# Optimization experiments

Measured on AMD Instinct MI355X. Metric: run time of the kernel, lower is better.

Reference implementation:

```python
import jax, jax.numpy as jnp
import numpy as np

P, M, N, H, B, E, K = 50, 512, 1024, 256, 8, 400, 5
ALPHA_MAX, TAU_MAX, RHO_MAX, ETA_MAX = 0.01, 1.0, 1.0, 1.0
LEAK = 0.01  # F.leaky_relu default slope


def _lrelu(x):
    return jnp.where(x >= 0, x, LEAK * x)


def _layernorm(x, g, b, eps=1e-5):
    mu = jnp.mean(x, axis=-1, keepdims=True)
    var = jnp.mean((x - mu) ** 2, axis=-1, keepdims=True)
    return (x - mu) * jax.lax.rsqrt(var + eps) * g + b


def setup_inputs() -> dict:
    ks = iter(jax.random.split(jax.random.key(0), 16))

    def w(fin, fout):
        return jax.random.normal(next(ks), (fin, fout), jnp.float32) * np.float32(np.sqrt(2.0 / (fin + fout)))

    H4 = 4 * H
    inp = {
        'A': jax.random.normal(next(ks), (1, P, M, N), jnp.float32) * 0.05,
        'b': jax.random.normal(next(ks), (B, P, M, 1), jnp.float32),
        'W1': w(2 * N, H), 'b1': jnp.zeros(H), 'bn1_s': jnp.ones(H), 'bn1_t': jnp.zeros(H),
        'W2': w(H, 2 * H), 'b2': jnp.zeros(2 * H), 'bn2_s': jnp.ones(2 * H), 'bn2_t': jnp.zeros(2 * H),
        'W3': w(2 * H, H4), 'b3': jnp.zeros(H4), 'bn3_s': jnp.ones(H4), 'bn3_t': jnp.zeros(H4),
        'W4': w(H4, H4), 'b4': jnp.zeros(H4), 'bn4_s': jnp.ones(H4), 'bn4_t': jnp.zeros(H4),
        'W5': w(H4, H4), 'b5': jnp.zeros(H4), 'bn5_s': jnp.ones(H4), 'bn5_t': jnp.zeros(H4),
        'ln_g': jnp.ones(H4), 'ln_b': jnp.zeros(H4),
        'Wd1': w(P * H4, H4), 'bd1': jnp.zeros(H4), 'lnd1_g': jnp.ones(H4), 'lnd1_b': jnp.zeros(H4),
        'Wd2': w(H4, 2 * H), 'bd2': jnp.zeros(2 * H), 'lnd2_g': jnp.ones(2 * H), 'lnd2_b': jnp.zeros(2 * H),
        'Wd3': w(2 * H, H), 'bd3': jnp.zeros(H), 'lnd3_g': jnp.ones(H), 'lnd3_b': jnp.zeros(H),
        'Wfc': w(H, 4) * 0.1, 'bfc': jnp.zeros(4),
        'edge_index': jax.random.randint(next(ks), (2, E), 0, P),
    }
    return inp


def reference(A, b, W1, b1, bn1_s, bn1_t, W2, b2, bn2_s, bn2_t, W3, b3, bn3_s, bn3_t,
              W4, b4, bn4_s, bn4_t, W5, b5, bn5_s, bn5_t, ln_g, ln_b,
              Wd1, bd1, lnd1_g, lnd1_b, Wd2, bd2, lnd2_g, lnd2_b, Wd3, bd3, lnd3_g, lnd3_b,
              Wfc, bfc, edge_index):
    A0 = A[0]                                             # [P,M,N]
    AtA = jnp.einsum('pmi,pmj->pij', A0, A0)              # [P,N,N]  (compute_Atx(A))
    Atb = jnp.einsum('pmn,bpm->bpn', A0, b[..., 0])[..., None]  # [B,P,N,1]

    src, dst = edge_index[0], edge_index[1]
    ones_e = jnp.ones((E,), A.dtype)
    # sum_neighbors: out-degree of each node p, shape broadcastable to [B,P,1,1]
    sum_nb = jax.ops.segment_sum(ones_e, src, num_segments=P)[None, :, None, None]

    # GCNConv normalization with self loops: norm_ij = deg_i^-1/2 * deg_j^-1/2
    sl = jnp.arange(P)
    src_a = jnp.concatenate([src, sl])
    dst_a = jnp.concatenate([dst, sl])
    deg = jax.ops.segment_sum(jnp.ones((E + P,), A.dtype), dst_a, num_segments=P)
    dinv = jax.lax.rsqrt(deg)
    coef = (dinv[src_a] * dinv[dst_a])[:, None]           # [E+P,1]

    convs = [(W1, b1, bn1_s, bn1_t), (W2, b2, bn2_s, bn2_t), (W3, b3, bn3_s, bn3_t),
             (W4, b4, bn4_s, bn4_t), (W5, b5, bn5_s, bn5_t)]

    def gconv(x, W, bias):                                # x: [P,Cin]
        xw = x @ W
        return jax.ops.segment_sum(xw[src_a] * coef, dst_a, num_segments=P) + bias

    def encode_one(feat):                                 # feat: [P,2N]
        x = feat
        for (W, bias, s, t) in convs:
            # leaky_relu -> BatchNorm1d (eval: affine scale/shift) -> dropout (eval: id)
            x = _lrelu(gconv(x, W, bias)) * s + t
        return _layernorm(x, ln_g, ln_b).reshape(-1)      # [P*4H]

    enc = jax.vmap(encode_one)

    y = jnp.zeros((B, P, N, 1), A.dtype)
    U = jnp.zeros_like(y)
    delta = jnp.zeros_like(y)
    Ys = []
    for k in range(K):
        AtAy = jnp.einsum('pij,bpj->bpi', AtA, y[..., 0])[..., None]  # [B,P,N,1]
        feat = jnp.concatenate([AtAy, Atb], axis=2)[..., 0]           # [B,P,2N]
        code = enc(feat)                                              # [B,P*4H]
        h = _lrelu(_layernorm(code @ Wd1 + bd1, lnd1_g, lnd1_b))
        h = _lrelu(_layernorm(h @ Wd2 + bd2, lnd2_g, lnd2_b))
        h = _lrelu(_layernorm(h @ Wd3 + bd3, lnd3_g, lnd3_b))
        hyp = jnp.clip(jax.nn.sigmoid(h @ Wfc + bfc), 1e-4, 0.99).reshape(B, 4, 1, 1, 1)
        alpha = hyp[:, 0] * ALPHA_MAX
        tau = hyp[:, 1] * TAU_MAX
        rho = hyp[:, 2] * RHO_MAX
        eta = hyp[:, 3] * ETA_MAX
        g = AtAy - Atb + jnp.sign(y) * tau + U * sum_nb + delta * rho
        mg = max(30.0, 100.0 - k)
        g = jnp.clip(g, -mg, mg)
        mv = max(10.0, 200.0 - k * 3)
        y = jnp.clip(y - alpha * g, -mv, mv)
        # compute_delta: for each directed edge (s,d): delta[s]+= (y_s-y_d); delta[d]-= (y_s-y_d)
        diff = y[:, src] - y[:, dst]                                  # [B,E,N,1]
        delta = jnp.zeros_like(y).at[:, src].add(diff).at[:, dst].add(-diff)
        U = jnp.clip(U + delta * eta, -mv, mv)
        Ys.append(y)
    return jnp.stack(Ys)                                              # [K,B,P,N,1]
```

## Files before the change

kernel.cpp:

```cpp
#include <hip/hip_runtime.h>

#define PP 50
#define MM 512
#define NN 1024

constexpr size_t F_ATB   = 0;
constexpr size_t F_ATAY  = F_ATB   + 409600;
constexpr size_t F_Y     = F_ATAY  + 409600;
constexpr size_t F_U     = F_Y     + 409600;
constexpr size_t F_DELTA = F_U     + 409600;
constexpr size_t F_BT    = F_DELTA + 409600;
constexpr size_t F_AYT   = F_BT    + 204800;
constexpr size_t F_ZA    = F_AYT   + 204800;
constexpr size_t F_ZB    = F_ZA    + 458752;
constexpr size_t F_X0    = F_ZB    + 458752;
constexpr size_t F_X1    = F_X0    + 409600;
constexpr size_t F_CODET = F_X1    + 409600;
constexpr size_t F_PART  = F_CODET + 409600;
constexpr size_t F_DPART2= F_PART  + 3670016;
constexpr size_t F_H1    = F_DPART2+ 32768;
constexpr size_t F_H2    = F_H1    + 8192;
constexpr size_t F_H3    = F_H2    + 4096;
constexpr size_t F_HYP   = F_H3    + 2048;
constexpr size_t F_GCCO  = F_HYP   + 64;
constexpr size_t F_SUMNB = F_GCCO  + 512;
constexpr size_t F_END   = F_SUMNB + 64;

__device__ __forceinline__ float lrelu(float v) { return v >= 0.f ? v : 0.01f * v; }

__device__ __forceinline__ void bred2(float& s1, float& s2, float* sm) {
  #pragma unroll
  for (int off = 32; off > 0; off >>= 1) {
    s1 += __shfl_down(s1, off);
    s2 += __shfl_down(s2, off);
  }
  int w = threadIdx.x >> 6, l = threadIdx.x & 63;
  if (l == 0) { sm[w] = s1; sm[4 + w] = s2; }
  __syncthreads();
  s1 = sm[0] + sm[1] + sm[2] + sm[3];
  s2 = sm[4] + sm[5] + sm[6] + sm[7];
}

__global__ __launch_bounds__(512) void ksetup(const int* __restrict__ ei, float* sumnb,
                                              float* gccoef, int* gcoff, int* gcsrc,
                                              int* nbroff, int* nbridx) {
  __shared__ int cin[PP];
  __shared__ int cou[PP];
  __shared__ float sdinv[PP];
  __shared__ int goff[PP + 1], noff[PP + 1];
  int t = threadIdx.x;
  const int* src = ei;
  const int* dst = ei + 400;
  if (t < PP) { cin[t] = 0; cou[t] = 0; }
  __syncthreads();
  if (t < 400) {
    atomicAdd(&cou[src[t]], 1);
    atomicAdd(&cin[dst[t]], 1);
  }
  __syncthreads();
  if (t < PP) {
    sdinv[t] = rsqrtf((float)(cin[t] + 1));
    sumnb[t] = (float)cou[t];
  }
  __syncthreads();
  if (t == 0) {
    goff[0] = 0; noff[0] = 0;
    for (int p = 0; p < PP; ++p) {
      goff[p + 1] = goff[p] + cin[p] + 1;
      noff[p + 1] = noff[p] + cin[p] + cou[p];
    }
  }
  __syncthreads();
  if (t <= PP) { gcoff[t] = goff[t]; nbroff[t] = noff[t]; }
  if (t < 400) {
    int d = dst[t], s = src[t];
    int slot = 0;
    for (int e = 0; e < t; ++e) slot += (dst[e] == d) ? 1 : 0;
    int pos = goff[d] + slot;
    gcsrc[pos] = s;
    gccoef[pos] = sdinv[s] * sdinv[d];
  }
  if (t < PP) {
    int pos = goff[t] + cin[t];
    gcsrc[pos] = t;
    gccoef[pos] = sdinv[t] * sdinv[t];
  }
  if (t < 400) {
    int s = src[t], d = dst[t];
    int so = 0, si = 0;
    for (int e = 0; e < t; ++e) {
      so += (src[e] == s) ? 1 : 0;
      si += (dst[e] == d) ? 1 : 0;
    }
    nbridx[noff[s] + so] = d;
    nbridx[noff[d] + cou[d] + si] = s;
  }
}

__global__ __launch_bounds__(256) void kbt(const float* __restrict__ b, float* __restrict__ bt) {
  int i = blockIdx.x * 256 + threadIdx.x;
  int bb = i / (PP * MM);
  int r = i - bb * (PP * MM);
  bt[r * 8 + bb] = b[i];
}

__global__ __launch_bounds__(256) void katz(const float* __restrict__ A, const float* __restrict__ q,
                                            float* __restrict__ outv) {
  __shared__ float red[4][64][8];
  int nb = blockIdx.x, p = blockIdx.y, t = threadIdx.x;
  int ln = t & 63, mg = t >> 6;
  int n = nb * 64 + ln;
  float acc[8] = {0, 0, 0, 0, 0, 0, 0, 0};
  const float* ap = A + ((size_t)p * MM + mg * 128) * NN + n;
  const float* qp = q + ((size_t)p * MM + mg * 128) * 8;
  for (int m0 = 0; m0 < 128; m0 += 8) {
    float av[8];
    #pragma unroll
    for (int u = 0; u < 8; ++u) av[u] = ap[(size_t)(m0 + u) * NN];
    #pragma unroll
    for (int u = 0; u < 8; ++u) {
      #pragma unroll
      for (int bb = 0; bb < 8; ++bb) acc[bb] += av[u] * qp[(m0 + u) * 8 + bb];
    }
  }
  #pragma unroll
  for (int bb = 0; bb < 8; ++bb) red[mg][ln][bb] = acc[bb];
  __syncthreads();
  if (mg == 0) {
    #pragma unroll
    for (int bb = 0; bb < 8; ++bb) {
      float v = red[0][ln][bb] + red[1][ln][bb] + red[2][ln][bb] + red[3][ln][bb];
      outv[((size_t)bb * PP + p) * NN + n] = v;
    }
  }
}

__global__ __launch_bounds__(256) void kay(const float* __restrict__ A, const float* __restrict__ y,
                                           float* __restrict__ ayt) {
  __shared__ __align__(16) float sy[8][NN];
  int p = blockIdx.x, mb = blockIdx.y, t = threadIdx.x;
  #pragma unroll
  for (int bb = 0; bb < 8; ++bb)
    for (int n = t; n < NN; n += 256) sy[bb][n] = y[(bb * PP + p) * NN + n];
  __syncthreads();
  int w = t >> 6, l = t & 63;
  int mbase = mb * 64 + w * 16;
  for (int i = 0; i < 8; ++i) {
    int m0 = mbase + 2 * i, m1 = m0 + 1;
    float acc0[8] = {0, 0, 0, 0, 0, 0, 0, 0};
    float acc1[8] = {0, 0, 0, 0, 0, 0, 0, 0};
    const float* a0p = A + ((size_t)p * MM + m0) * NN;
    const float* a1p = a0p + NN;
    #pragma unroll
    for (int jj = 0; jj < 4; ++jj) {
      int n0 = 4 * l + 256 * jj;
      float4 a0 = *(const float4*)(a0p + n0);
      float4 a1 = *(const float4*)(a1p + n0);
      #pragma unroll
      for (int bb = 0; bb < 8; ++bb) {
        float4 yv = *(const float4*)&sy[bb][n0];
        acc0[bb] += a0.x * yv.x + a0.y * yv.y + a0.z * yv.z + a0.w * yv.w;
        acc1[bb] += a1.x * yv.x + a1.y * yv.y + a1.z * yv.z + a1.w * yv.w;
      }
    }
    #pragma unroll
    for (int off = 32; off > 0; off >>= 1) {
      #pragma unroll
      for (int bb = 0; bb < 8; ++bb) {
        acc0[bb] += __shfl_down(acc0[bb], off);
        acc1[bb] += __shfl_down(acc1[bb], off);
      }
    }
    if (l == 0) {
      #pragma unroll
      for (int bb = 0; bb < 8; ++bb) {
        ayt[((size_t)p * MM + m0) * 8 + bb] = acc0[bb];
        ayt[((size_t)p * MM + m1) * 8 + bb] = acc1[bb];
      }
    }
  }
}

__global__ __launch_bounds__(256) void kgatherX(const float* __restrict__ x, float* __restrict__ z,
                                                int Cin, const int* __restrict__ gcoff,
                                                const int* __restrict__ gcsrc,
                                                const float* __restrict__ gccoef) {
  int r = blockIdx.x, cc = blockIdx.y, t = threadIdx.x;
  int c = cc * 256 + t;
  size_t zi = (size_t)r * Cin + c;
  if (r >= 400) { z[zi] = 0.f; return; }
  int b = r / 50, p = r - b * 50;
  float acc = 0.f;
  int o0 = gcoff[p], o1 = gcoff[p + 1];
  for (int idx = o0; idx < o1; ++idx)
    acc += gccoef[idx] * x[((size_t)b * 50 + gcsrc[idx]) * Cin + c];
  z[zi] = acc;
}

__global__ __launch_bounds__(256) void kgemm(const float* __restrict__ X, const float* __restrict__ W,
                                             float* __restrict__ part, int K, int C, int krange) {
  int cb = blockIdx.x, rb = blockIdx.y, s = blockIdx.z;
  int t = threadIdx.x;
  __shared__ __align__(16) float As[16][64];
  __shared__ __align__(16) float Bs[16][68];
  int rbase = rb * 64, cbase = cb * 64;
  int k0 = s * krange, kend = k0 + krange;
  float acc[4][4] = {};
  int tx = t & 15, ty = t >> 4;
  int lrow = t >> 2, lk = (t & 3) * 4;
  int brow = t >> 4, bc = (t & 15) * 4;
  for (int k = k0; k < kend; k += 16) {
    float4 av = *(const float4*)(X + (size_t)(rbase + lrow) * K + k + lk);
    As[lk + 0][lrow] = av.x;
    As[lk + 1][lrow] = av.y;
    As[lk + 2][lrow] = av.z;
    As[lk + 3][lrow] = av.w;
    *(float4*)&Bs[brow][bc] = *(const float4*)(W + (size_t)(k + brow) * C + cbase + bc);
    __syncthreads();
    #pragma unroll
    for (int kk = 0; kk < 16; ++kk) {
      float4 a = *(const float4*)&As[kk][ty * 4];
      float4 b = *(const float4*)&Bs[kk][tx * 4];
      float aa[4] = {a.x, a.y, a.z, a.w};
      float bb[4] = {b.x, b.y, b.z, b.w};
      #pragma unroll
      for (int i = 0; i < 4; ++i)
        #pragma unroll
        for (int j = 0; j < 4; ++j) acc[i][j] += aa[i] * bb[j];
    }
    __syncthreads();
  }
  #pragma unroll
  for (int i = 0; i < 4; ++i) {
    int r = rbase + ty * 4 + i;
    *(float4*)&part[((size_t)s * 448 + r) * C + cbase + tx * 4] =
        make_float4(acc[i][0], acc[i][1], acc[i][2], acc[i][3]);
  }
}

__global__ __launch_bounds__(256) void kgemmC(const float* __restrict__ XA, const float* __restrict__ XB,
                                              const float* __restrict__ W, float* __restrict__ part,
                                              int C, int krange, int koff) {
  int cb = blockIdx.x, rb = blockIdx.y, s = blockIdx.z;
  int t = threadIdx.x;
  __shared__ __align__(16) float As[16][64];
  __shared__ __align__(16) float Bs[16][68];
  int rbase = rb * 64, cbase = cb * 64;
  int k0 = koff + s * krange, kend = k0 + krange;
  float acc[4][4] = {};
  int tx = t & 15, ty = t >> 4;
  int lrow = t >> 2, lk = (t & 3) * 4;
  int brow = t >> 4, bc = (t & 15) * 4;
  for (int k = k0; k < kend; k += 16) {
    int r = rbase + lrow;
    const float* xp = (k < 1024) ? (XA + (size_t)r * 1024 + k)
                                 : (XB + (size_t)r * 1024 + (k - 1024));
    float4 av = *(const float4*)(xp + lk);
    As[lk + 0][lrow] = av.x;
    As[lk + 1][lrow] = av.y;
    As[lk + 2][lrow] = av.z;
    As[lk + 3][lrow] = av.w;
    *(float4*)&Bs[brow][bc] = *(const float4*)(W + (size_t)(k + brow) * C + cbase + bc);
    __syncthreads();
    #pragma unroll
    for (int kk = 0; kk < 16; ++kk) {
      float4 a = *(const float4*)&As[kk][ty * 4];
      float4 b = *(const float4*)&Bs[kk][tx * 4];
      float aa[4] = {a.x, a.y, a.z, a.w};
      float bb[4] = {b.x, b.y, b.z, b.w};
      #pragma unroll
      for (int i = 0; i < 4; ++i)
        #pragma unroll
        for (int j = 0; j < 4; ++j) acc[i][j] += aa[i] * bb[j];
    }
    __syncthreads();
  }
  #pragma unroll
  for (int i = 0; i < 4; ++i) {
    int r = rbase + ty * 4 + i;
    *(float4*)&part[((size_t)s * 448 + r) * C + cbase + tx * 4] =
        make_float4(acc[i][0], acc[i][1], acc[i][2], acc[i][3]);
  }
}

template <int NCH, bool LASTLN>
__global__ __launch_bounds__(256) void kredE(const float* __restrict__ part, int S,
                                             const float* __restrict__ bias,
                                             const float* __restrict__ bns,
                                             const float* __restrict__ bnt,
                                             float* __restrict__ xout,
                                             const float* __restrict__ lng,
                                             const float* __restrict__ lnb,
                                             float* __restrict__ codet) {
  __shared__ float smr[8];
  constexpr int C = NCH * 256;
  int r = blockIdx.x, t = threadIdx.x;
  float vals[NCH];
  #pragma unroll
  for (int ch = 0; ch < NCH; ++ch) {
    int c = ch * 256 + t;
    float acc = 0.f;
    const float* pp = part + (size_t)r * C + c;
    #pragma unroll 4
    for (int s = 0; s < S; ++s) acc += pp[(size_t)s * 448 * C];
    float v = lrelu(acc + bias[c]);
    vals[ch] = v * bns[c] + bnt[c];
  }
  if (!LASTLN) {
    #pragma unroll
    for (int ch = 0; ch < NCH; ++ch)
      xout[(size_t)r * C + ch * 256 + t] = vals[ch];
  } else {
    float s1 = 0.f, s2 = 0.f;
    #pragma unroll
    for (int ch = 0; ch < NCH; ++ch) { s1 += vals[ch]; s2 += vals[ch] * vals[ch]; }
    bred2(s1, s2, smr);
    float mu = s1 / (float)C;
    float var = s2 / (float)C - mu * mu;
    float rs = rsqrtf(var + 1e-5f);
    int b = r / 50, p = r - b * 50;
    #pragma unroll
    for (int ch = 0; ch < NCH; ++ch) {
      int c = ch * 256 + t;
      codet[((size_t)p * C + c) * 8 + b] = (vals[ch] - mu) * rs * lng[c] + lnb[c];
    }
  }
}

__global__ __launch_bounds__(256) void kwd1(const float* __restrict__ W,
                                            const float* __restrict__ in_t,
                                            float* __restrict__ dpart) {
  int t = threadIdx.x, s = blockIdx.x;
  int k0 = s * 200;
  float4 acc[8];
  #pragma unroll
  for (int b = 0; b < 8; ++b) acc[b] = make_float4(0.f, 0.f, 0.f, 0.f);
  const float* wp = W + (size_t)k0 * 1024 + 4 * t;
  const float* qp = in_t + (size_t)k0 * 8;
  for (int k = 0; k < 200; k += 4) {
    float4 wv[4], qa[4], qb[4];
    #pragma unroll
    for (int u = 0; u < 4; ++u) {
      wv[u] = *(const float4*)(wp + (size_t)(k + u) * 1024);
      qa[u] = *(const float4*)(qp + (k + u) * 8);
      qb[u] = *(const float4*)(qp + (k + u) * 8 + 4);
    }
    #pragma unroll
    for (int u = 0; u < 4; ++u) {
      float qs[8] = {qa[u].x, qa[u].y, qa[u].z, qa[u].w, qb[u].x, qb[u].y, qb[u].z, qb[u].w};
      #pragma unroll
      for (int b = 0; b < 8; ++b) {
        acc[b].x += wv[u].x * qs[b];
        acc[b].y += wv[u].y * qs[b];
        acc[b].z += wv[u].z * qs[b];
        acc[b].w += wv[u].w * qs[b];
      }
    }
  }
  #pragma unroll
  for (int b = 0; b < 8; ++b)
    *(float4*)&dpart[(size_t)(s * 8 + b) * 1024 + 4 * t] = acc[b];
}

__global__ __launch_bounds__(256) void kredA(const float* __restrict__ dpart,
                                             float* __restrict__ dpart2) {
  int cb = blockIdx.x, sg = blockIdx.y, b = blockIdx.z, t = threadIdx.x;
  int c = cb * 256 + t;
  float acc = 0.f;
  const float* pp = dpart + ((size_t)(sg * 64) * 8 + b) * 1024 + c;
  #pragma unroll 8
  for (int i = 0; i < 64; ++i) acc += pp[(size_t)i * 8 * 1024];
  dpart2[((size_t)sg * 8 + b) * 1024 + c] = acc;
}

__global__ __launch_bounds__(128) void kwdS(const float* __restrict__ W,
                                            const float* __restrict__ in_t,
                                            float* __restrict__ part, int C, int krange) {
  int t = threadIdx.x, s = blockIdx.x;
  int k0 = s * krange;
  float4 acc[8];
  #pragma unroll
  for (int b = 0; b < 8; ++b) acc[b] = make_float4(0.f, 0.f, 0.f, 0.f);
  const float* wp = W + (size_t)k0 * C + 4 * t;
  const float* qp = in_t + (size_t)k0 * 8;
  for (int k = 0; k < krange; ++k) {
    float4 wv = *(const float4*)(wp + (size_t)k * C);
    float4 qa = *(const float4*)(qp + k * 8);
    float4 qb = *(const float4*)(qp + k * 8 + 4);
    float qs[8] = {qa.x, qa.y, qa.z, qa.w, qb.x, qb.y, qb.z, qb.w};
    #pragma unroll
    for (int b = 0; b < 8; ++b) {
      acc[b].x += wv.x * qs[b];
      acc[b].y += wv.y * qs[b];
      acc[b].z += wv.z * qs[b];
      acc[b].w += wv.w * qs[b];
    }
  }
  #pragma unroll
  for (int b = 0; b < 8; ++b)
    *(float4*)&part[(size_t)(s * 8 + b) * C + 4 * t] = acc[b];
}

__global__ __launch_bounds__(1024) void kred(const float* __restrict__ part, int S, int C,
                                             const float* __restrict__ bias,
                                             const float* __restrict__ g,
                                             const float* __restrict__ be,
                                             float* __restrict__ out_t) {
  __shared__ float sm[32];
  int b = blockIdx.x, t = threadIdx.x;
  float v = bias[t];
  const float* pp = part + (size_t)b * C + t;
  #pragma unroll 4
  for (int s = 0; s < S; ++s) v += pp[(size_t)s * 8 * C];
  float s1 = v, s2 = v * v;
  #pragma unroll
  for (int off = 32; off > 0; off >>= 1) {
    s1 += __shfl_down(s1, off);
    s2 += __shfl_down(s2, off);
  }
  int w = t >> 6, l = t & 63;
  int nw = blockDim.x >> 6;
  if (l == 0) { sm[w] = s1; sm[16 + w] = s2; }
  __syncthreads();
  s1 = 0.f; s2 = 0.f;
  for (int i = 0; i < nw; ++i) { s1 += sm[i]; s2 += sm[16 + i]; }
  float inv = 1.f / (float)C;
  float mu = s1 * inv;
  float var = s2 * inv - mu * mu;
  float rs = rsqrtf(var + 1e-5f);
  float o = lrelu((v - mu) * rs * g[t] + be[t]);
  out_t[t * 8 + b] = o;
}

__global__ __launch_bounds__(256) void kwfc(const float* __restrict__ Wfc, const float* __restrict__ bfc,
                                            const float* __restrict__ h3t, float* __restrict__ hyp) {
  __shared__ float sd[32][257];
  int t = threadIdx.x;
  float4 w = *(const float4*)(Wfc + t * 4);
  #pragma unroll
  for (int bb = 0; bb < 8; ++bb) {
    float x = h3t[t * 8 + bb];
    sd[bb * 4 + 0][t] = x * w.x;
    sd[bb * 4 + 1][t] = x * w.y;
    sd[bb * 4 + 2][t] = x * w.z;
    sd[bb * 4 + 3][t] = x * w.w;
  }
  __syncthreads();
  if (t < 32) {
    float s = 0.f;
    for (int i = 0; i < 256; ++i) s += sd[t][i];
    s += bfc[t & 3];
    float sig = 1.f / (1.f + expf(-s));
    sig = fminf(fmaxf(sig, 1e-4f), 0.99f);
    hyp[t] = sig;
  }
}

__global__ __launch_bounds__(256) void kyupd(const float* __restrict__ atay, const float* __restrict__ atb,
                                             float* y, const float* __restrict__ U,
                                             const float* __restrict__ delta,
                                             const float* __restrict__ hyp,
                                             const float* __restrict__ sumnb, float* __restrict__ outp,
                                             float mg, float mv, int first) {
  int i = blockIdx.x * 256 + threadIdx.x;
  int bb = i / (PP * NN);
  int rem = i - bb * (PP * NN);
  int p = rem >> 10;
  float alpha = hyp[bb * 4 + 0] * 0.01f;
  float g, yv;
  if (first) {
    yv = 0.f;
    g = -atb[i];
  } else {
    float tau = hyp[bb * 4 + 1];
    float rho = hyp[bb * 4 + 2];
    yv = y[i];
    float sg = (yv > 0.f) ? 1.f : ((yv < 0.f) ? -1.f : 0.f);
    g = atay[i] - atb[i] + sg * tau + U[i] * sumnb[p] + delta[i] * rho;
  }
  g = fminf(fmaxf(g, -mg), mg);
  float yn = yv - alpha * g;
  yn = fminf(fmaxf(yn, -mv), mv);
  y[i] = yn;
  outp[i] = yn;
}

__global__ __launch_bounds__(256) void kdeltaU(const float* __restrict__ y, float* __restrict__ delta,
                                               float* __restrict__ U, const float* __restrict__ hyp,
                                               const int* __restrict__ nbroff,
                                               const int* __restrict__ nbridx, float mv, int first) {
  int t = threadIdx.x;
  int n = blockIdx.x * 256 + t;
  int p = blockIdx.y;
  int bb = blockIdx.z;
  int o0 = nbroff[p], o1 = nbroff[p + 1];
  int base = bb * (PP * NN) + p * NN;
  float d = (float)(o1 - o0) * y[base + n];
  for (int idx = o0; idx < o1; ++idx) {
    int q = nbridx[idx];
    d -= y[bb * (PP * NN) + q * NN + n];
  }
  delta[base + n] = d;
  float eta = hyp[bb * 4 + 3];
  float u0 = first ? 0.f : U[base + n];
  float u = u0 + d * eta;
  U[base + n] = fminf(fmaxf(u, -mv), mv);
}

extern "C" void kernel_launch(void* const* d_in, const int* in_sizes, int n_in,
                              void* d_out, int out_size, void* d_ws, size_t ws_size,
                              hipStream_t stream) {
  const float* A    = (const float*)d_in[0];
  const float* bvec = (const float*)d_in[1];
  const float* W1 = (const float*)d_in[2];
  const float* b1 = (const float*)d_in[3];
  const float* bn1s = (const float*)d_in[4];
  const float* bn1t = (const float*)d_in[5];
  const float* W2 = (const float*)d_in[6];
  const float* b2 = (const float*)d_in[7];
  const float* bn2s = (const float*)d_in[8];
  const float* bn2t = (const float*)d_in[9];
  const float* W3 = (const float*)d_in[10];
  const float* b3 = (const float*)d_in[11];
  const float* bn3s = (const float*)d_in[12];
  const float* bn3t = (const float*)d_in[13];
  const float* W4 = (const float*)d_in[14];
  const float* b4 = (const float*)d_in[15];
  const float* bn4s = (const float*)d_in[16];
  const float* bn4t = (const float*)d_in[17];
  const float* W5 = (const float*)d_in[18];
  const float* b5 = (const float*)d_in[19];
  const float* bn5s = (const float*)d_in[20];
  const float* bn5t = (const float*)d_in[21];
  const float* lng = (const float*)d_in[22];
  const float* lnb = (const float*)d_in[23];
  const float* Wd1 = (const float*)d_in[24];
  const float* bd1 = (const float*)d_in[25];
  const float* lnd1g = (const float*)d_in[26];
  const float* lnd1b = (const float*)d_in[27];
  const float* Wd2 = (const float*)d_in[28];
  const float* bd2 = (const float*)d_in[29];
  const float* lnd2g = (const float*)d_in[30];
  const float* lnd2b = (const float*)d_in[31];
  const float* Wd3 = (const float*)d_in[32];
  const float* bd3 = (const float*)d_in[33];
  const float* lnd3g = (const float*)d_in[34];
  const float* lnd3b = (const float*)d_in[35];
  const float* Wfc = (const float*)d_in[36];
  const float* bfc = (const float*)d_in[37];
  const int* ei = (const int*)d_in[38];

  float* out = (float*)d_out;
  float* wsf = (float*)d_ws;
  float* atb = wsf + F_ATB;
  float* atay = wsf + F_ATAY;
  float* yb = wsf + F_Y;
  float* Ub = wsf + F_U;
  float* db = wsf + F_DELTA;
  float* bt = wsf + F_BT;
  float* ayt = wsf + F_AYT;
  float* zA = wsf + F_ZA;
  float* zB = wsf + F_ZB;
  float* x0 = wsf + F_X0;
  float* x1 = wsf + F_X1;
  float* codet = wsf + F_CODET;
  float* part = wsf + F_PART;
  float* dpart = part;
  float* dpart2 = wsf + F_DPART2;
  float* h1t = wsf + F_H1;
  float* h2t = wsf + F_H2;
  float* h3t = wsf + F_H3;
  float* hyp = wsf + F_HYP;
  float* gccoef = wsf + F_GCCO;
  float* sumnb = wsf + F_SUMNB;
  int* wsi = (int*)(wsf + F_END);
  int* gcoff = wsi;
  int* gcsrc = wsi + 64;
  int* nbroff = wsi + 576;
  int* nbridx = wsi + 640;

  ksetup<<<1, 512, 0, stream>>>(ei, sumnb, gccoef, gcoff, gcsrc, nbroff, nbridx);
  kbt<<<800, 256, 0, stream>>>(bvec, bt);
  katz<<<dim3(16, 50), 256, 0, stream>>>(A, bt, atb);
  kgatherX<<<dim3(448, 4), 256, 0, stream>>>(atb, zB, 1024, gcoff, gcsrc, gccoef);

  const float mgs[5] = {100.f, 99.f, 98.f, 97.f, 96.f};
  const float mvs[5] = {200.f, 197.f, 194.f, 191.f, 188.f};

  for (int k = 0; k < 5; ++k) {
    if (k > 0) {
      kay<<<dim3(50, 8), 256, 0, stream>>>(A, yb, ayt);
      katz<<<dim3(16, 50), 256, 0, stream>>>(A, ayt, atay);
    }
    if (k == 0) {
      kgemmC<<<dim3(4, 7, 4), 256, 0, stream>>>(zA, zB, W1, part, 256, 256, 1024);
      kredE<1, false><<<400, 256, 0, stream>>>(part, 4, b1, bn1s, bn1t, x0, nullptr, nullptr, nullptr);
    } else {
      kgatherX<<<dim3(448, 4), 256, 0, stream>>>(atay, zA, 1024, gcoff, gcsrc, gccoef);
      kgemmC<<<dim3(4, 7, 8), 256, 0, stream>>>(zA, zB, W1, part, 256, 256, 0);
      kredE<1, false><<<400, 256, 0, stream>>>(part, 8, b1, bn1s, bn1t, x0, nullptr, nullptr, nullptr);
    }
    kgatherX<<<dim3(448, 1), 256, 0, stream>>>(x0, zA, 256, gcoff, gcsrc, gccoef);
    kgemm<<<dim3(8, 7, 4), 256, 0, stream>>>(zA, W2, part, 256, 512, 64);
    kredE<2, false><<<400, 256, 0, stream>>>(part, 4, b2, bn2s, bn2t, x1, nullptr, nullptr, nullptr);
    kgatherX<<<dim3(448, 2), 256, 0, stream>>>(x1, zA, 512, gcoff, gcsrc, gccoef);
    kgemm<<<dim3(16, 7, 4), 256, 0, stream>>>(zA, W3, part, 512, 1024, 128);
    kredE<4, false><<<400, 256, 0, stream>>>(part, 4, b3, bn3s, bn3t, x0, nullptr, nullptr, nullptr);
    kgatherX<<<dim3(448, 4), 256, 0, stream>>>(x0, zA, 1024, gcoff, gcsrc, gccoef);
    kgemm<<<dim3(16, 7, 4), 256, 0, stream>>>(zA, W4, part, 1024, 1024, 256);
    kredE<4, false><<<400, 256, 0, stream>>>(part, 4, b4, bn4s, bn4t, x1, nullptr, nullptr, nullptr);
    kgatherX<<<dim3(448, 4), 256, 0, stream>>>(x1, zA, 1024, gcoff, gcsrc, gccoef);
    kgemm<<<dim3(16, 7, 4), 256, 0, stream>>>(zA, W5, part, 1024, 1024, 256);
    kredE<4, true><<<400, 256, 0, stream>>>(part, 4, b5, bn5s, bn5t, nullptr, lng, lnb, codet);
    kwd1<<<256, 256, 0, stream>>>(Wd1, codet, dpart);
    kredA<<<dim3(4, 4, 8), 256, 0, stream>>>(dpart, dpart2);
    kred<<<8, 1024, 0, stream>>>(dpart2, 4, 1024, bd1, lnd1g, lnd1b, h1t);
    kwdS<<<64, 128, 0, stream>>>(Wd2, h1t, dpart, 512, 16);
    kred<<<8, 512, 0, stream>>>(dpart, 64, 512, bd2, lnd2g, lnd2b, h2t);
    kwdS<<<32, 64, 0, stream>>>(Wd3, h2t, dpart, 256, 16);
    kred<<<8, 256, 0, stream>>>(dpart, 32, 256, bd3, lnd3g, lnd3b, h3t);
    kwfc<<<1, 256, 0, stream>>>(Wfc, bfc, h3t, hyp);
    kyupd<<<1600, 256, 0, stream>>>(atay, atb, yb, Ub, db, hyp, sumnb,
                                    out + (size_t)k * 409600, mgs[k], mvs[k], k == 0);
    kdeltaU<<<dim3(4, 50, 8), 256, 0, stream>>>(yb, db, Ub, hyp, nbroff, nbridx, mvs[k], k == 0);
  }
}
```

Baseline: 1.591 ms.

## Fuse A·y and Aᵀ(Ay) into a single pass over A per iteration

Replaces the two-kernel sequence (kay computing A·y, then katz computing Aᵀ·(Ay)) with one kernel that streams each row chunk of A once. For each group of four rows it forms the dot products with y, reduces them across the block, then accumulates the row times that scalar into Aᵀ·(Ay). The M dimension is split into four chunks whose partial results go to a buffer, and a small kernel sums them. This halves reads of the large A tensor per iteration, at the cost of two block barriers per four rows, only 200 blocks of parallelism, and an extra partial-sum buffer.

```diff
diff --git a/kernel.cpp b/kernel.cpp
--- a/kernel.cpp
+++ b/kernel.cpp
@@ -135,50 +135,67 @@
   }
 }
 
-__global__ __launch_bounds__(256) void kay(const float* __restrict__ A, const float* __restrict__ y,
-                                           float* __restrict__ ayt) {
-  __shared__ __align__(16) float sy[8][NN];
-  int p = blockIdx.x, mb = blockIdx.y, t = threadIdx.x;
-  #pragma unroll
-  for (int bb = 0; bb < 8; ++bb)
-    for (int n = t; n < NN; n += 256) sy[bb][n] = y[(bb * PP + p) * NN + n];
-  __syncthreads();
+__global__ __launch_bounds__(256) void katay(const float* __restrict__ A,
+                                             const float* __restrict__ y,
+                                             float* __restrict__ part) {
+  __shared__ float sred[4][4][8];
+  int mg = blockIdx.x, p = blockIdx.y, t = threadIdx.x;
   int w = t >> 6, l = t & 63;
-  int mbase = mb * 64 + w * 16;
-  for (int i = 0; i < 8; ++i) {
-    int m0 = mbase + 2 * i, m1 = m0 + 1;
-    float acc0[8] = {0, 0, 0, 0, 0, 0, 0, 0};
-    float acc1[8] = {0, 0, 0, 0, 0, 0, 0, 0};
-    const float* a0p = A + ((size_t)p * MM + m0) * NN;
-    const float* a1p = a0p + NN;
-    #pragma unroll
-    for (int jj = 0; jj < 4; ++jj) {
-      int n0 = 4 * l + 256 * jj;
-      float4 a0 = *(const float4*)(a0p + n0);
-      float4 a1 = *(const float4*)(a1p + n0);
-      #pragma unroll
-      for (int bb = 0; bb < 8; ++bb) {
-        float4 yv = *(const float4*)&sy[bb][n0];
-        acc0[bb] += a0.x * yv.x + a0.y * yv.y + a0.z * yv.z + a0.w * yv.w;
-        acc1[bb] += a1.x * yv.x + a1.y * yv.y + a1.z * yv.z + a1.w * yv.w;
+  int c4 = 4 * t;
+  float4 yq[8];
+  #pragma unroll
+  for (int b = 0; b < 8; ++b)
+    yq[b] = *(const float4*)(y + ((size_t)b * PP + p) * NN + c4);
+  float4 acc[8];
+  #pragma unroll
+  for (int b = 0; b < 8; ++b) acc[b] = make_float4(0.f, 0.f, 0.f, 0.f);
+  const float* ap = A + ((size_t)p * MM + mg * 128) * NN + c4;
+  for (int m0 = 0; m0 < 128; m0 += 4) {
+    float4 av[4];
+    #pragma unroll
+    for (int u = 0; u < 4; ++u) av[u] = *(const float4*)(ap + (size_t)(m0 + u) * NN);
+    float d[4][8];
+    #pragma unroll
+    for (int u = 0; u < 4; ++u)
+      #pragma unroll
+      for (int b = 0; b < 8; ++b)
+        d[u][b] = av[u].x * yq[b].x + av[u].y * yq[b].y + av[u].z * yq[b].z + av[u].w * yq[b].w;
+    #pragma unroll
+    for (int off = 32; off > 0; off >>= 1)
+      #pragma unroll
+      for (int u = 0; u < 4; ++u)
+        #pragma unroll
+        for (int b = 0; b < 8; ++b) d[u][b] += __shfl_down(d[u][b], off);
+    if (l == 0) {
+      #pragma unroll
+      for (int u = 0; u < 4; ++u)
+        #pragma unroll
+        for (int b = 0; b < 8; ++b) sred[u][w][b] = d[u][b];
+    }
+    __syncthreads();
+    #pragma unroll
+    for (int u = 0; u < 4; ++u) {
+      #pragma unroll
+      for (int b = 0; b < 8; ++b) {
+        float s = sred[u][0][b] + sred[u][1][b] + sred[u][2][b] + sred[u][3][b];
+        acc[b].x += s * av[u].x;
+        acc[b].y += s * av[u].y;
+        acc[b].z += s * av[u].z;
+        acc[b].w += s * av[u].w;
       }
     }
-    #pragma unroll
-    for (int off = 32; off > 0; off >>= 1) {
-      #pragma unroll
-      for (int bb = 0; bb < 8; ++bb) {
-        acc0[bb] += __shfl_down(acc0[bb], off);
-        acc1[bb] += __shfl_down(acc1[bb], off);
-      }
-    }
-    if (l == 0) {
-      #pragma unroll
-      for (int bb = 0; bb < 8; ++bb) {
-        ayt[((size_t)p * MM + m0) * 8 + bb] = acc0[bb];
-        ayt[((size_t)p * MM + m1) * 8 + bb] = acc1[bb];
-      }
-    }
-  }
+    __syncthreads();
+  }
+  #pragma unroll
+  for (int b = 0; b < 8; ++b)
+    *(float4*)&part[(((size_t)mg * 8 + b) * PP + p) * NN + c4] = acc[b];
+}
+
+__global__ __launch_bounds__(256) void kredAtay(const float* __restrict__ part,
+                                                float* __restrict__ atay) {
+  int i = blockIdx.x * 256 + threadIdx.x;
+  float v = part[i] + part[409600 + i] + part[2 * 409600 + i] + part[3 * 409600 + i];
+  atay[i] = v;
 }
 
 __global__ __launch_bounds__(256) void kgatherX(const float* __restrict__ x, float* __restrict__ z,
@@ -558,7 +575,6 @@
   float* Ub = wsf + F_U;
   float* db = wsf + F_DELTA;
   float* bt = wsf + F_BT;
-  float* ayt = wsf + F_AYT;
   float* zA = wsf + F_ZA;
   float* zB = wsf + F_ZB;
   float* x0 = wsf + F_X0;
@@ -589,8 +605,8 @@
 
   for (int k = 0; k < 5; ++k) {
     if (k > 0) {
-      kay<<<dim3(50, 8), 256, 0, stream>>>(A, yb, ayt);
-      katz<<<dim3(16, 50), 256, 0, stream>>>(A, ayt, atay);
+      katay<<<dim3(4, 50), 256, 0, stream>>>(A, yb, part);
+      kredAtay<<<1600, 256, 0, stream>>>(part, atay);
     }
     if (k == 0) {
       kgemmC<<<dim3(4, 7, 4), 256, 0, stream>>>(zA, zB, W1, part, 256, 256, 1024);
```

After: 1.773 ms. +11.5%, slower.
